# Kernel optimization log

Hardware: AMD Instinct MI355X
Metric: run time of the kernel (lower is better)

The kernel has to match this reference:

```python
import jax, jax.numpy as jnp
import numpy as np

B, S, D, H = 64, 512, 1024, 1024

def setup_inputs() -> dict:
    key = jax.random.key(0)
    k1, k2, k3 = jax.random.split(key, 3)
    inp = jax.random.normal(k1, (B, S, D), dtype=jnp.float32)
    # gate order: i, f, o, c_hat ; Wx ~ fc1.weight (no bias), Wh ~ fc2.weight, b ~ fc2.bias
    Wx = jax.random.normal(k2, (4, H, D), dtype=jnp.float32) * 0.02
    Wh = jax.random.normal(k3, (4, H, H), dtype=jnp.float32) * 0.02
    b = jnp.zeros((4, H), dtype=jnp.float32)
    return {"input": inp, "Wx": Wx, "Wh": Wh, "b": b}

def reference(input, Wx, Wh, b):
    # Precompute all input projections for all 4 gates in one big GEMM:
    # (S, B, 4, H) with time leading for scan
    x_proj = jnp.einsum('bsd,ghd->sbgh', input, Wx)

    def step(carry, xp):
        h, c = carry
        # hidden projections for all 4 gates: one batched GEMM per step
        g = xp + jnp.einsum('bh,gkh->bgk', h, Wh) + b  # (B, 4, H)
        i_t = jax.nn.sigmoid(g[:, 0])
        f_t = jax.nn.sigmoid(g[:, 1])
        o_t = jax.nn.sigmoid(g[:, 2])
        c_hat = jnp.tanh(g[:, 3])
        c_new = f_t * c + i_t * c_hat
        h_new = o_t * jnp.tanh(c_new)
        return (h_new, c_new), h_new

    h0 = jnp.zeros((input.shape[0], Wh.shape[-1]), dtype=input.dtype)
    c0 = jnp.zeros_like(h0)
    (h_last, c_last), ys = jax.lax.scan(step, (h0, c0), x_proj)
    output = jnp.transpose(ys, (1, 0, 2))  # (B, S, H)
    return output, (h_last, c_last)
```

## Files before the change

### kernel.cpp

```cpp
#include <hip/hip_runtime.h>

#define B_ 64
#define S_ 512
#define D_ 1024
#define H_ 1024
#define NBLK 256
#define NT 256
#define TB 8

typedef __bf16 v8bf __attribute__((ext_vector_type(8)));
typedef float v4f __attribute__((ext_vector_type(4)));
typedef float f32x4 __attribute__((ext_vector_type(4)));
typedef unsigned long long u64;

__device__ inline v8bf cvt8(const float* p) {
  f32x4 a = *(const f32x4*)p;
  f32x4 b = *(const f32x4*)(p + 4);
  v8bf r;
  r[0] = (__bf16)a[0]; r[1] = (__bf16)a[1]; r[2] = (__bf16)a[2]; r[3] = (__bf16)a[3];
  r[4] = (__bf16)b[0]; r[5] = (__bf16)b[1]; r[6] = (__bf16)b[2]; r[7] = (__bf16)b[3];
  return r;
}

__global__ __launch_bounds__(NT, 1)
void lstm_persist(const float* __restrict__ x,
                  const float* __restrict__ Wx,
                  const float* __restrict__ Wh,
                  const float* __restrict__ bias,
                  float* __restrict__ out,
                  __bf16* __restrict__ hblk,
                  unsigned* __restrict__ flags)
{
  __shared__ v8bf wlds[16 * 256];

  const int tid  = threadIdx.x;
  const int nb   = blockIdx.x;
  const int w    = tid >> 6;
  const int l    = tid & 63;
  const int lm   = l & 15;
  const int quad = l >> 4;
  const int sw   = lm & 7;

  for (int i = tid; i < 16 * 256; i += NT) {
    const int nl  = i >> 8;
    const int kc  = i & 255;
    const int g   = nl >> 2;
    const int col = (nb << 2) + (nl & 3);
    const int k   = kc << 3;
    const float* src = (k < D_)
        ? (Wx + ((size_t)(g * H_ + col) * D_ + k))
        : (Wh + ((size_t)(g * H_ + col) * H_ + (k - D_)));
    wlds[(nl << 8) + (kc ^ (nl & 7))] = cvt8(src);
  }

  const int myb   = (w << 4) + lm;
  const int myb4  = myb << 2;
  const int mycol = (nb << 2) + quad;
  float bv[4];
  #pragma unroll
  for (int g = 0; g < 4; ++g) bv[g] = bias[g * H_ + mycol];

  float c_reg = 0.f;
  float obuf[TB];

  const unsigned* fw     = flags + (w << 8);
  unsigned*       myflag = flags + (w << 8) + nb;

  __syncthreads();

  for (int t = 0; t < S_; ++t) {
    v4f acc[2];
    acc[0] = (v4f){0.f, 0.f, 0.f, 0.f};
    acc[1] = (v4f){0.f, 0.f, 0.f, 0.f};

    const float* xrow = x + ((size_t)(myb * S_ + t)) * D_ + (quad << 3);
    #pragma unroll 4
    for (int qq = 0; qq < 16; ++qq) {
      const int q0 = qq * 2, q1 = qq * 2 + 1;
      v8bf a0 = cvt8(xrow + (q0 << 5));
      v8bf b0 = wlds[(lm << 8) + (((q0 << 2) + quad) ^ sw)];
      acc[0] = __builtin_amdgcn_mfma_f32_16x16x32_bf16(a0, b0, acc[0], 0, 0, 0);
      v8bf a1 = cvt8(xrow + (q1 << 5));
      v8bf b1 = wlds[(lm << 8) + (((q1 << 2) + quad) ^ sw)];
      acc[1] = __builtin_amdgcn_mfma_f32_16x16x32_bf16(a1, b1, acc[1], 0, 0, 0);
    }

    if (t > 0) {
      const unsigned tu = (unsigned)t;
      for (;;) {
        const unsigned f0 = __hip_atomic_load(fw + (l << 2) + 0,
            __ATOMIC_RELAXED, __HIP_MEMORY_SCOPE_AGENT);
        const unsigned f1 = __hip_atomic_load(fw + (l << 2) + 1,
            __ATOMIC_RELAXED, __HIP_MEMORY_SCOPE_AGENT);
        const unsigned f2 = __hip_atomic_load(fw + (l << 2) + 2,
            __ATOMIC_RELAXED, __HIP_MEMORY_SCOPE_AGENT);
        const unsigned f3 = __hip_atomic_load(fw + (l << 2) + 3,
            __ATOMIC_RELAXED, __HIP_MEMORY_SCOPE_AGENT);
        if (__all((f0 >= tu) & (f1 >= tu) & (f2 >= tu) & (f3 >= tu))) break;
        __builtin_amdgcn_s_sleep(1);
      }
      asm volatile("" ::: "memory");

      const __bf16* hb = hblk + ((t & 1) ? (1 << 16) : 0);
      #pragma unroll 4
      for (int c = 0; c < 32; ++c) {
        const int j0 = (quad << 1) + (c << 3);
        union { u64 q[2]; v8bf v; } a;
        a.q[0] = __hip_atomic_load((const u64*)(hb + (j0 << 8) + myb4),
            __ATOMIC_RELAXED, __HIP_MEMORY_SCOPE_AGENT);
        a.q[1] = __hip_atomic_load((const u64*)(hb + ((j0 + 1) << 8) + myb4),
            __ATOMIC_RELAXED, __HIP_MEMORY_SCOPE_AGENT);
        v8bf b = wlds[(lm << 8) + ((128 + (c << 2) + quad) ^ sw)];
        acc[c & 1] = __builtin_amdgcn_mfma_f32_16x16x32_bf16(a.v, b, acc[c & 1], 0, 0, 0);
      }
    }

    v4f accs = acc[0] + acc[1];

    float gv[4];
    const int rsel = lm & 3;
    #pragma unroll
    for (int g = 0; g < 4; ++g) {
      const int srcl = ((lm >> 2) << 4) + (g << 2) + quad;
      float t0 = __shfl(accs[0], srcl, 64);
      float t1 = __shfl(accs[1], srcl, 64);
      float t2 = __shfl(accs[2], srcl, 64);
      float t3 = __shfl(accs[3], srcl, 64);
      gv[g] = (rsel == 0 ? t0 : rsel == 1 ? t1 : rsel == 2 ? t2 : t3) + bv[g];
    }

    const float it = 1.f / (1.f + __expf(-gv[0]));
    const float ft = 1.f / (1.f + __expf(-gv[1]));
    const float ot = 1.f / (1.f + __expf(-gv[2]));
    const float ch = 1.f - 2.f / (__expf(2.f * gv[3]) + 1.f);
    c_reg = ft * c_reg + it * ch;
    const float hn = ot * (1.f - 2.f / (__expf(2.f * c_reg) + 1.f));

    {
      union { __bf16 b; unsigned short s; } hb2;
      hb2.b = (__bf16)hn;
      __hip_atomic_store(
          (unsigned short*)(hblk + (((t + 1) & 1) ? (1 << 16) : 0)
                            + (nb << 8) + myb4 + quad),
          hb2.s, __ATOMIC_RELAXED, __HIP_MEMORY_SCOPE_AGENT);
    }

    asm volatile("s_waitcnt vmcnt(0)" ::: "memory");
    __hip_atomic_store(myflag, (unsigned)(t + 1), __ATOMIC_RELAXED,
                       __HIP_MEMORY_SCOPE_AGENT);

    obuf[t & (TB - 1)] = hn;
    if ((t & (TB - 1)) == TB - 1) {
      #pragma unroll
      for (int i = 0; i < TB; ++i)
        __builtin_nontemporal_store(
            obuf[i], &out[((size_t)(myb * S_ + (t - TB + 1 + i))) * H_ + mycol]);
    }
    if (t == S_ - 1) {
      __builtin_nontemporal_store(
          hn, &out[(size_t)B_ * S_ * H_ + (size_t)myb * H_ + mycol]);
      __builtin_nontemporal_store(
          c_reg, &out[(size_t)B_ * S_ * H_ + (size_t)(B_ * H_)
                      + (size_t)myb * H_ + mycol]);
    }
  }
}

extern "C" void kernel_launch(void* const* d_in, const int* in_sizes, int n_in,
                              void* d_out, int out_size, void* d_ws, size_t ws_size,
                              hipStream_t stream) {
  const float* x    = (const float*)d_in[0];
  const float* Wx   = (const float*)d_in[1];
  const float* Wh   = (const float*)d_in[2];
  const float* bias = (const float*)d_in[3];
  float* out = (float*)d_out;

  unsigned* flags = (unsigned*)d_ws;
  __bf16*   hblk  = (__bf16*)((char*)d_ws + 4096);

  hipMemsetAsync(d_ws, 0, 4096, stream);

  lstm_persist<<<dim3(NBLK), dim3(NT), 0, stream>>>(x, Wx, Wh, bias, out, hblk,
                                                    flags);
}
```

Before: 7.102 ms.

## Split block into producer waves for input projection and consumer waves for recurrence

Doubles the block to 512 threads. Four producer waves compute the x·Wx projection for upcoming timesteps into a 4-slot LDS ring buffer, and four consumer waves run the recurrent h·Wh step, gates and the global flag synchronisation. Workgroup-scope sequence counters in LDS coordinate the two groups. The aim is to take the input-projection GEMM and its global x loads off the serial critical path so they overlap with waiting on the grid-wide h exchange. It uses more LDS, needs a dynamic shared-memory size above 64KB, and adds intra-block spin-waits.

```diff
diff --git a/kernel.cpp b/kernel.cpp
--- a/kernel.cpp
+++ b/kernel.cpp
@@ -5,13 +5,17 @@
 #define D_ 1024
 #define H_ 1024
 #define NBLK 256
-#define NT 256
+#define NT 512
 #define TB 8
+#define NSLOT 4
 
 typedef __bf16 v8bf __attribute__((ext_vector_type(8)));
 typedef float v4f __attribute__((ext_vector_type(4)));
 typedef float f32x4 __attribute__((ext_vector_type(4)));
 typedef unsigned long long u64;
+typedef unsigned u32;
+
+#define MFMA __builtin_amdgcn_mfma_f32_16x16x32_bf16
 
 __device__ inline v8bf cvt8(const float* p) {
   f32x4 a = *(const f32x4*)p;
@@ -22,20 +26,23 @@
   return r;
 }
 
-__global__ __launch_bounds__(NT, 1)
+__global__ __launch_bounds__(NT, 2)
 void lstm_persist(const float* __restrict__ x,
                   const float* __restrict__ Wx,
                   const float* __restrict__ Wh,
                   const float* __restrict__ bias,
                   float* __restrict__ out,
                   __bf16* __restrict__ hblk,
-                  unsigned* __restrict__ flags)
+                  u32* __restrict__ flags)
 {
-  __shared__ v8bf wlds[16 * 256];
+  extern __shared__ char smem[];
+  v8bf* wlds = (v8bf*)smem;
+  v4f*  xacc = (v4f*)(smem + 65536);
+  u32*  seq  = (u32*)(smem + 65536 + 16384);
 
   const int tid  = threadIdx.x;
   const int nb   = blockIdx.x;
-  const int w    = tid >> 6;
+  const int w8   = tid >> 6;
   const int l    = tid & 63;
   const int lm   = l & 15;
   const int quad = l >> 4;
@@ -52,116 +59,152 @@
         : (Wh + ((size_t)(g * H_ + col) * H_ + (k - D_)));
     wlds[(nl << 8) + (kc ^ (nl & 7))] = cvt8(src);
   }
-
-  const int myb   = (w << 4) + lm;
-  const int myb4  = myb << 2;
-  const int mycol = (nb << 2) + quad;
-  float bv[4];
-  #pragma unroll
-  for (int g = 0; g < 4; ++g) bv[g] = bias[g * H_ + mycol];
-
-  float c_reg = 0.f;
-  float obuf[TB];
-
-  const unsigned* fw     = flags + (w << 8);
-  unsigned*       myflag = flags + (w << 8) + nb;
+  if (tid < 128) seq[tid] = 0;
 
   __syncthreads();
 
-  for (int t = 0; t < S_; ++t) {
-    v4f acc[2];
-    acc[0] = (v4f){0.f, 0.f, 0.f, 0.f};
-    acc[1] = (v4f){0.f, 0.f, 0.f, 0.f};
-
-    const float* xrow = x + ((size_t)(myb * S_ + t)) * D_ + (quad << 3);
-    #pragma unroll 4
-    for (int qq = 0; qq < 16; ++qq) {
-      const int q0 = qq * 2, q1 = qq * 2 + 1;
-      v8bf a0 = cvt8(xrow + (q0 << 5));
-      v8bf b0 = wlds[(lm << 8) + (((q0 << 2) + quad) ^ sw)];
-      acc[0] = __builtin_amdgcn_mfma_f32_16x16x32_bf16(a0, b0, acc[0], 0, 0, 0);
-      v8bf a1 = cvt8(xrow + (q1 << 5));
-      v8bf b1 = wlds[(lm << 8) + (((q1 << 2) + quad) ^ sw)];
-      acc[1] = __builtin_amdgcn_mfma_f32_16x16x32_bf16(a1, b1, acc[1], 0, 0, 0);
+  u32* xseq = seq;
+  u32* hseq = seq + 64;
+
+  if (w8 < 4) {
+    const int w   = w8;
+    const int myb = (w << 4) + lm;
+    for (int t = 0; t < S_; ++t) {
+      if (t >= NSLOT) {
+        while (__hip_atomic_load(&hseq[w << 4], __ATOMIC_ACQUIRE,
+                                 __HIP_MEMORY_SCOPE_WORKGROUP)
+               < (u32)(t - NSLOT + 1)) {
+          __builtin_amdgcn_s_sleep(1);
+        }
+      }
+      v4f a0 = {0.f,0.f,0.f,0.f}, a1 = {0.f,0.f,0.f,0.f};
+      const float* xrow = x + ((size_t)(myb * S_ + t)) * D_ + (quad << 3);
+      #pragma unroll 4
+      for (int cc = 0; cc < 16; ++cc) {
+        const int c0 = cc * 2, c1 = cc * 2 + 1;
+        v8bf f0 = cvt8(xrow + (c0 << 5));
+        a0 = MFMA(f0, wlds[(lm << 8) + (((c0 << 2) + quad) ^ sw)], a0, 0, 0, 0);
+        v8bf f1 = cvt8(xrow + (c1 << 5));
+        a1 = MFMA(f1, wlds[(lm << 8) + (((c1 << 2) + quad) ^ sw)], a1, 0, 0, 0);
+      }
+      xacc[((t & (NSLOT - 1)) << 8) + (w << 6) + l] = a0 + a1;
+      asm volatile("s_waitcnt lgkmcnt(0)" ::: "memory");
+      if (l == 0)
+        __hip_atomic_store(&xseq[w << 4], (u32)(t + 1), __ATOMIC_RELEASE,
+                           __HIP_MEMORY_SCOPE_WORKGROUP);
     }
-
-    if (t > 0) {
-      const unsigned tu = (unsigned)t;
-      for (;;) {
-        const unsigned f0 = __hip_atomic_load(fw + (l << 2) + 0,
-            __ATOMIC_RELAXED, __HIP_MEMORY_SCOPE_AGENT);
-        const unsigned f1 = __hip_atomic_load(fw + (l << 2) + 1,
-            __ATOMIC_RELAXED, __HIP_MEMORY_SCOPE_AGENT);
-        const unsigned f2 = __hip_atomic_load(fw + (l << 2) + 2,
-            __ATOMIC_RELAXED, __HIP_MEMORY_SCOPE_AGENT);
-        const unsigned f3 = __hip_atomic_load(fw + (l << 2) + 3,
-            __ATOMIC_RELAXED, __HIP_MEMORY_SCOPE_AGENT);
-        if (__all((f0 >= tu) & (f1 >= tu) & (f2 >= tu) & (f3 >= tu))) break;
+  } else {
+    const int s     = w8 & 3;
+    const int myb   = (s << 4) + lm;
+    const int myb4  = myb << 2;
+    const int mycol = (nb << 2) + quad;
+    float bv[4];
+    #pragma unroll
+    for (int g = 0; g < 4; ++g) bv[g] = bias[g * H_ + mycol];
+
+    float c_reg = 0.f;
+    float obuf[TB];
+
+    const u32* fw     = flags + (s << 8);
+    u32*       myflag = flags + (s << 8) + nb;
+
+    for (int t = 0; t < S_; ++t) {
+      while (__hip_atomic_load(&xseq[s << 4], __ATOMIC_ACQUIRE,
+                               __HIP_MEMORY_SCOPE_WORKGROUP) < (u32)(t + 1)) {
         __builtin_amdgcn_s_sleep(1);
       }
-      asm volatile("" ::: "memory");
-
-      const __bf16* hb = hblk + ((t & 1) ? (1 << 16) : 0);
-      #pragma unroll 4
-      for (int c = 0; c < 32; ++c) {
-        const int j0 = (quad << 1) + (c << 3);
-        union { u64 q[2]; v8bf v; } a;
-        a.q[0] = __hip_atomic_load((const u64*)(hb + (j0 << 8) + myb4),
-            __ATOMIC_RELAXED, __HIP_MEMORY_SCOPE_AGENT);
-        a.q[1] = __hip_atomic_load((const u64*)(hb + ((j0 + 1) << 8) + myb4),
-            __ATOMIC_RELAXED, __HIP_MEMORY_SCOPE_AGENT);
-        v8bf b = wlds[(lm << 8) + ((128 + (c << 2) + quad) ^ sw)];
-        acc[c & 1] = __builtin_amdgcn_mfma_f32_16x16x32_bf16(a.v, b, acc[c & 1], 0, 0, 0);
-      }
-    }
-
-    v4f accs = acc[0] + acc[1];
-
-    float gv[4];
-    const int rsel = lm & 3;
-    #pragma unroll
-    for (int g = 0; g < 4; ++g) {
-      const int srcl = ((lm >> 2) << 4) + (g << 2) + quad;
-      float t0 = __shfl(accs[0], srcl, 64);
-      float t1 = __shfl(accs[1], srcl, 64);
-      float t2 = __shfl(accs[2], srcl, 64);
-      float t3 = __shfl(accs[3], srcl, 64);
-      gv[g] = (rsel == 0 ? t0 : rsel == 1 ? t1 : rsel == 2 ? t2 : t3) + bv[g];
-    }
-
-    const float it = 1.f / (1.f + __expf(-gv[0]));
-    const float ft = 1.f / (1.f + __expf(-gv[1]));
-    const float ot = 1.f / (1.f + __expf(-gv[2]));
-    const float ch = 1.f - 2.f / (__expf(2.f * gv[3]) + 1.f);
-    c_reg = ft * c_reg + it * ch;
-    const float hn = ot * (1.f - 2.f / (__expf(2.f * c_reg) + 1.f));
-
-    {
-      union { __bf16 b; unsigned short s; } hb2;
-      hb2.b = (__bf16)hn;
-      __hip_atomic_store(
-          (unsigned short*)(hblk + (((t + 1) & 1) ? (1 << 16) : 0)
-                            + (nb << 8) + myb4 + quad),
-          hb2.s, __ATOMIC_RELAXED, __HIP_MEMORY_SCOPE_AGENT);
-    }
-
-    asm volatile("s_waitcnt vmcnt(0)" ::: "memory");
-    __hip_atomic_store(myflag, (unsigned)(t + 1), __ATOMIC_RELAXED,
-                       __HIP_MEMORY_SCOPE_AGENT);
-
-    obuf[t & (TB - 1)] = hn;
-    if ((t & (TB - 1)) == TB - 1) {
+      const v4f xa = xacc[((t & (NSLOT - 1)) << 8) + (s << 6) + l];
+      asm volatile("s_waitcnt lgkmcnt(0)" ::: "memory");
+      if (l == 0)
+        __hip_atomic_store(&hseq[s << 4], (u32)(t + 1), __ATOMIC_RELEASE,
+                           __HIP_MEMORY_SCOPE_WORKGROUP);
+
+      v4f acc0 = xa, acc1 = {0.f,0.f,0.f,0.f};
+
+      if (t > 0) {
+        const u32 tu = (u32)t;
+        for (;;) {
+          const u32 f0 = __hip_atomic_load(fw + (l << 2) + 0,
+              __ATOMIC_RELAXED, __HIP_MEMORY_SCOPE_AGENT);
+          const u32 f1 = __hip_atomic_load(fw + (l << 2) + 1,
+              __ATOMIC_RELAXED, __HIP_MEMORY_SCOPE_AGENT);
+          const u32 f2 = __hip_atomic_load(fw + (l << 2) + 2,
+              __ATOMIC_RELAXED, __HIP_MEMORY_SCOPE_AGENT);
+          const u32 f3 = __hip_atomic_load(fw + (l << 2) + 3,
+              __ATOMIC_RELAXED, __HIP_MEMORY_SCOPE_AGENT);
+          if (__all((f0 >= tu) & (f1 >= tu) & (f2 >= tu) & (f3 >= tu))) break;
+          __builtin_amdgcn_s_sleep(1);
+        }
+        asm volatile("" ::: "memory");
+
+        const __bf16* hb = hblk + ((t & 1) ? (1 << 16) : 0);
+        #pragma unroll 4
+        for (int cc = 0; cc < 16; ++cc) {
+          const int c0 = cc * 2, c1 = cc * 2 + 1;
+          const int j0 = (quad << 1) + (c0 << 3);
+          const int j1 = (quad << 1) + (c1 << 3);
+          union { u64 q[2]; v8bf v; } h0, h1;
+          h0.q[0] = __hip_atomic_load((const u64*)(hb + (j0 << 8) + myb4),
+              __ATOMIC_RELAXED, __HIP_MEMORY_SCOPE_AGENT);
+          h0.q[1] = __hip_atomic_load((const u64*)(hb + ((j0 + 1) << 8) + myb4),
+              __ATOMIC_RELAXED, __HIP_MEMORY_SCOPE_AGENT);
+          h1.q[0] = __hip_atomic_load((const u64*)(hb + (j1 << 8) + myb4),
+              __ATOMIC_RELAXED, __HIP_MEMORY_SCOPE_AGENT);
+          h1.q[1] = __hip_atomic_load((const u64*)(hb + ((j1 + 1) << 8) + myb4),
+              __ATOMIC_RELAXED, __HIP_MEMORY_SCOPE_AGENT);
+          acc0 = MFMA(h0.v, wlds[(lm << 8) + ((128 + (c0 << 2) + quad) ^ sw)], acc0, 0, 0, 0);
+          acc1 = MFMA(h1.v, wlds[(lm << 8) + ((128 + (c1 << 2) + quad) ^ sw)], acc1, 0, 0, 0);
+        }
+      }
+
+      v4f accs = acc0 + acc1;
+
+      float gv[4];
+      const int rsel = lm & 3;
       #pragma unroll
-      for (int i = 0; i < TB; ++i)
+      for (int g = 0; g < 4; ++g) {
+        const int srcl = ((lm >> 2) << 4) + (g << 2) + quad;
+        float t0 = __shfl(accs[0], srcl, 64);
+        float t1 = __shfl(accs[1], srcl, 64);
+        float t2 = __shfl(accs[2], srcl, 64);
+        float t3 = __shfl(accs[3], srcl, 64);
+        gv[g] = (rsel == 0 ? t0 : rsel == 1 ? t1 : rsel == 2 ? t2 : t3) + bv[g];
+      }
+
+      const float it = 1.f / (1.f + __expf(-gv[0]));
+      const float ft = 1.f / (1.f + __expf(-gv[1]));
+      const float ot = 1.f / (1.f + __expf(-gv[2]));
+      const float ch = 1.f - 2.f / (__expf(2.f * gv[3]) + 1.f);
+      c_reg = ft * c_reg + it * ch;
+      const float hn = ot * (1.f - 2.f / (__expf(2.f * c_reg) + 1.f));
+
+      {
+        union { __bf16 b; unsigned short u; } hb2;
+        hb2.b = (__bf16)hn;
+        __hip_atomic_store(
+            (unsigned short*)(hblk + (((t + 1) & 1) ? (1 << 16) : 0)
+                              + (nb << 8) + myb4 + quad),
+            hb2.u, __ATOMIC_RELAXED, __HIP_MEMORY_SCOPE_AGENT);
+      }
+
+      asm volatile("s_waitcnt vmcnt(0)" ::: "memory");
+      __hip_atomic_store(myflag, (u32)(t + 1), __ATOMIC_RELAXED,
+                         __HIP_MEMORY_SCOPE_AGENT);
+
+      obuf[t & (TB - 1)] = hn;
+      if ((t & (TB - 1)) == TB - 1) {
+        #pragma unroll
+        for (int i = 0; i < TB; ++i)
+          __builtin_nontemporal_store(
+              obuf[i], &out[((size_t)(myb * S_ + (t - TB + 1 + i))) * H_ + mycol]);
+      }
+      if (t == S_ - 1) {
         __builtin_nontemporal_store(
-            obuf[i], &out[((size_t)(myb * S_ + (t - TB + 1 + i))) * H_ + mycol]);
-    }
-    if (t == S_ - 1) {
-      __builtin_nontemporal_store(
-          hn, &out[(size_t)B_ * S_ * H_ + (size_t)myb * H_ + mycol]);
-      __builtin_nontemporal_store(
-          c_reg, &out[(size_t)B_ * S_ * H_ + (size_t)(B_ * H_)
-                      + (size_t)myb * H_ + mycol]);
+            hn, &out[(size_t)B_ * S_ * H_ + (size_t)myb * H_ + mycol]);
+        __builtin_nontemporal_store(
+            c_reg, &out[(size_t)B_ * S_ * H_ + (size_t)(B_ * H_)
+                        + (size_t)myb * H_ + mycol]);
+      }
     }
   }
 }
@@ -175,11 +218,12 @@
   const float* bias = (const float*)d_in[3];
   float* out = (float*)d_out;
 
-  unsigned* flags = (unsigned*)d_ws;
-  __bf16*   hblk  = (__bf16*)((char*)d_ws + 4096);
+  u32*    flags = (u32*)d_ws;
+  __bf16* hblk  = (__bf16*)((char*)d_ws + 4096);
 
   hipMemsetAsync(d_ws, 0, 4096, stream);
 
-  lstm_persist<<<dim3(NBLK), dim3(NT), 0, stream>>>(x, Wx, Wh, bias, out, hblk,
-                                                    flags);
+  const size_t lds_bytes = 65536 + NSLOT * 4 * 64 * 16 + 512;
+  lstm_persist<<<dim3(NBLK), dim3(NT), lds_bytes, stream>>>(
+      x, Wx, Wh, bias, out, hblk, flags);
 }
```

After: 6.731 ms. 5.2% less time.
